# Optimization experiments

Measured on AMD Instinct MI355X. Metric: run time of the kernel, lower is better.

The kernel has to match this reference:

```python
import jax, jax.numpy as jnp
import numpy as np

N_NODES = 65536
N_EDGES = 1048576
VOCAB = 50000
HIDDEN = 256
LAYERS = 3
NUM_GRAPHS = 64
NEG_SLOPE = 0.2  # PyG GATConv default LeakyReLU slope
EPS = 1e-16      # PyG softmax denominator epsilon


def setup_inputs() -> dict:
    key = jax.random.key(0)
    ks = jax.random.split(key, 12)
    s = 0.02
    nodes = jax.random.randint(ks[0], (N_NODES,), 0, VOCAB, dtype=jnp.int32)
    edge_index = jax.random.randint(ks[1], (2, N_EDGES), 0, N_NODES, dtype=jnp.int32)
    batch = jnp.sort(jax.random.randint(ks[2], (N_NODES,), 0, NUM_GRAPHS, dtype=jnp.int32))
    emb = jax.random.normal(ks[3], (VOCAB, HIDDEN), jnp.float32) * s
    Wg = jax.random.normal(ks[4], (LAYERS, HIDDEN, HIDDEN), jnp.float32) * s
    a_src = jax.random.normal(ks[5], (LAYERS, HIDDEN), jnp.float32) * s
    a_dst = jax.random.normal(ks[6], (LAYERS, HIDDEN), jnp.float32) * s
    bg = jnp.zeros((LAYERS, HIDDEN), jnp.float32)
    Wl = jax.random.normal(ks[7], (LAYERS, HIDDEN, HIDDEN), jnp.float32) * s
    bl = jnp.zeros((LAYERS, HIDDEN), jnp.float32)
    Wout = jax.random.normal(ks[8], (HIDDEN, VOCAB), jnp.float32) * s
    bout = jnp.zeros((VOCAB,), jnp.float32)
    return {"nodes": nodes, "edge_index": edge_index, "batch": batch,
            "emb": emb, "Wg": Wg, "a_src": a_src, "a_dst": a_dst, "bg": bg,
            "Wl": Wl, "bl": bl, "Wout": Wout, "bout": bout}


def _gat_layer(x, src, dst, W, a_s, a_d, b, n):
    h = x @ W                                    # [N, H]
    e = jax.nn.leaky_relu((h @ a_s)[src] + (h @ a_d)[dst], NEG_SLOPE)  # [E]
    m = jax.ops.segment_max(e, dst, num_segments=n)
    w = jnp.exp(e - m[dst])
    denom = jax.ops.segment_sum(w, dst, num_segments=n)
    alpha = w / (denom[dst] + EPS)               # segment softmax over incoming edges
    out = jax.ops.segment_sum(h[src] * alpha[:, None], dst, num_segments=n)
    return out + b


def reference(nodes, edge_index, batch, emb, Wg, a_src, a_dst, bg, Wl, bl, Wout, bout):
    n = nodes.shape[0]
    loop = jnp.arange(n, dtype=edge_index.dtype)  # GATConv add_self_loops=True
    src = jnp.concatenate([edge_index[0], loop])
    dst = jnp.concatenate([edge_index[1], loop])
    x = emb[nodes]                                # [N, H]
    for l in range(Wg.shape[0]):
        x = _gat_layer(x, src, dst, Wg[l], a_src[l], a_dst[l], bg[l], n)
        x = jax.nn.relu(x)
        x = x @ Wl[l] + bl[l]
    sums = jax.ops.segment_sum(x, batch, num_segments=NUM_GRAPHS)
    cnt = jax.ops.segment_sum(jnp.ones((n,), x.dtype), batch, num_segments=NUM_GRAPHS)
    pooled = sums / jnp.maximum(cnt, 1.0)[:, None]  # global mean pool -> [G, H]
    return pooled @ Wout + bout                      # [G, V]
```

## Files before the change

### kernel.cpp

```cpp
#include <hip/hip_runtime.h>

#define N_NODES 65536
#define N_EDGES 1048576
#define E_TOTAL (N_EDGES + N_NODES)
#define VOCAB 50000
#define HIDDEN 256
#define NUM_GRAPHS 64
#define NEG_SLOPE 0.2f
#define SM_EPS 1e-16f

#define NBKT 128
#define BKT_SHIFT 9
#define DSTS_PER_BKT 512
#define BKT_CAP 10240
#define EDGES_PER_BLK1 4352

typedef _Float16 f16x8 __attribute__((ext_vector_type(8)));
typedef _Float16 f16x4 __attribute__((ext_vector_type(4)));
typedef float f32x4 __attribute__((ext_vector_type(4)));

__global__ __launch_bounds__(256) void gather_kernel(const int* __restrict__ nodes,
    const float* __restrict__ emb, _Float16* __restrict__ x) {
    int i = blockIdx.x;
    int t = threadIdx.x;
    x[(size_t)i * HIDDEN + t] = (_Float16)emb[(size_t)nodes[i] * HIDDEN + t];
}

__global__ __launch_bounds__(256) void prep_wt_kernel(const float* __restrict__ Wg,
    const float* __restrict__ Wl, _Float16* __restrict__ WT) {
    int mat = blockIdx.y;
    int n = blockIdx.x;
    int k = threadIdx.x;
    float s;
    if (mat == 0) {
        s = Wg[(size_t)k * HIDDEN + n];
    } else {
        const float* A = Wl + (size_t)(mat - 1) * HIDDEN * HIDDEN;
        const float* B = Wg + (size_t)mat * HIDDEN * HIDDEN;
        s = 0.f;
        for (int j = 0; j < HIDDEN; j++)
            s += A[(size_t)k * HIDDEN + j] * B[(size_t)j * HIDDEN + n];
    }
    WT[(size_t)mat * HIDDEN * HIDDEN + (size_t)n * HIDDEN + k] = (_Float16)s;
}

__global__ __launch_bounds__(256) void fuse_b_kernel(const float* __restrict__ Wg,
    const float* __restrict__ bl, float* __restrict__ bfused) {
    int pair = blockIdx.x;
    int n = threadIdx.x;
    const float* B = Wg + (size_t)(pair + 1) * HIDDEN * HIDDEN;
    const float* b = bl + (size_t)pair * HIDDEN;
    float s = 0.f;
    for (int k = 0; k < HIDDEN; k++) s += b[k] * B[(size_t)k * HIDDEN + n];
    bfused[pair * HIDDEN + n] = s;
}

__global__ __launch_bounds__(256) void bucket_kernel(const int* __restrict__ ei,
    int* __restrict__ bcur, unsigned* __restrict__ staging) {
    __shared__ int lhist[NBKT];
    __shared__ int lbase[NBKT];
    __shared__ int lcur[NBKT];
    int tid = threadIdx.x;
    if (tid < NBKT) lhist[tid] = 0;
    __syncthreads();
    int e0 = blockIdx.x * EDGES_PER_BLK1;
    int mySrc[17], myDst[17];
    #pragma unroll
    for (int k = 0; k < 17; k++) {
        int e = e0 + k * 256 + tid;
        int src, dst;
        if (e < N_EDGES) { src = ei[e]; dst = ei[N_EDGES + e]; }
        else             { src = dst = e - N_EDGES; }
        mySrc[k] = src; myDst[k] = dst;
        atomicAdd(&lhist[dst >> BKT_SHIFT], 1);
    }
    __syncthreads();
    if (tid < NBKT) {
        int c = lhist[tid];
        lbase[tid] = (c > 0) ? atomicAdd(&bcur[tid], c) : 0;
        lcur[tid] = 0;
    }
    __syncthreads();
    #pragma unroll
    for (int k = 0; k < 17; k++) {
        int b = myDst[k] >> BKT_SHIFT;
        int pos = lbase[b] + atomicAdd(&lcur[b], 1);
        staging[(size_t)b * BKT_CAP + pos] =
            ((unsigned)(myDst[k] & (DSTS_PER_BKT - 1)) << 16) | (unsigned)mySrc[k];
    }
}

__global__ __launch_bounds__(256) void csr_kernel(const int* __restrict__ bcur,
    const unsigned* __restrict__ staging, int* __restrict__ row_ptr,
    int* __restrict__ src_sorted) {
    __shared__ unsigned sedge[BKT_CAP];
    __shared__ int shist[DSTS_PER_BKT];
    __shared__ int sbase[DSTS_PER_BKT];
    __shared__ int spart[256];
    int b = blockIdx.x;
    int tid = threadIdx.x;
    int cnt = bcur[b];

    spart[tid] = (tid < NBKT && tid < b) ? bcur[tid] : 0;
    __syncthreads();
    for (int d = 128; d > 0; d >>= 1) {
        if (tid < d) spart[tid] += spart[tid + d];
        __syncthreads();
    }
    int base = spart[0];
    __syncthreads();

    shist[tid] = 0; shist[tid + 256] = 0;
    __syncthreads();
    for (int i = tid; i < cnt; i += 256) {
        unsigned v = staging[(size_t)b * BKT_CAP + i];
        sedge[i] = v;
        atomicAdd(&shist[v >> 16], 1);
    }
    __syncthreads();
    int p = shist[2 * tid] + shist[2 * tid + 1];
    spart[tid] = p;
    __syncthreads();
    for (int d = 1; d < 256; d <<= 1) {
        int v = (tid >= d) ? spart[tid - d] : 0;
        __syncthreads();
        spart[tid] += v;
        __syncthreads();
    }
    int epair = spart[tid] - p;
    sbase[2 * tid] = epair;
    sbase[2 * tid + 1] = epair + shist[2 * tid];
    __syncthreads();
    row_ptr[b * DSTS_PER_BKT + tid] = base + sbase[tid];
    row_ptr[b * DSTS_PER_BKT + 256 + tid] = base + sbase[256 + tid];
    shist[tid] = sbase[tid];
    shist[tid + 256] = sbase[tid + 256];
    __syncthreads();
    for (int i = tid; i < cnt; i += 256) {
        unsigned v = sedge[i];
        int d = v >> 16;
        int pos = atomicAdd(&shist[d], 1);
        src_sorted[base + pos] = (int)(v & 0xFFFFu);
    }
    if (b == NBKT - 1 && tid == 0) row_ptr[N_NODES] = E_TOTAL;
}

#define PAD_K 40
template <bool FUSED>
__global__ __launch_bounds__(256) void gemm_f16_kernel(const _Float16* __restrict__ A,
    const _Float16* __restrict__ WT, const float* __restrict__ bias,
    _Float16* __restrict__ C,
    const float* __restrict__ a_s, const float* __restrict__ a_d,
    float* __restrict__ es, float* __restrict__ ed) {
    __shared__ _Float16 As[64][PAD_K];
    __shared__ _Float16 Bs[256][PAD_K];
    int tid = threadIdx.x;
    int wave = tid >> 6;
    int lane = tid & 63;
    int quad = lane >> 4;
    int l16 = lane & 15;
    int m0 = blockIdx.x * 64;

    f32x4 acc[16];
    #pragma unroll
    for (int ct = 0; ct < 16; ct++) acc[ct] = (f32x4){0.f, 0.f, 0.f, 0.f};

    for (int k0 = 0; k0 < HIDDEN; k0 += 32) {
        __syncthreads();
        {
            int row = tid >> 2, q = tid & 3;
            *(f16x8*)&As[row][q * 8] =
                *(const f16x8*)(A + (size_t)(m0 + row) * HIDDEN + k0 + q * 8);
        }
        #pragma unroll
        for (int i = 0; i < 4; i++) {
            int c = tid + i * 256;
            int row = c >> 2, q = c & 3;
            *(f16x8*)&Bs[row][q * 8] =
                *(const f16x8*)(WT + (size_t)row * HIDDEN + k0 + q * 8);
        }
        __syncthreads();
        f16x8 a = *(const f16x8*)&As[wave * 16 + l16][quad * 8];
        #pragma unroll
        for (int ct = 0; ct < 16; ct++) {
            f16x8 b = *(const f16x8*)&Bs[ct * 16 + l16][quad * 8];
            acc[ct] = __builtin_amdgcn_mfma_f32_16x16x32_f16(a, b, acc[ct], 0, 0, 0);
        }
    }
    int rowbase = m0 + wave * 16 + quad * 4;
    #pragma unroll
    for (int ct = 0; ct < 16; ct++) {
        int col = ct * 16 + l16;
        float bv = (bias != nullptr) ? bias[col] : 0.f;
        #pragma unroll
        for (int r = 0; r < 4; r++) {
            float hv = acc[ct][r] + bv;
            acc[ct][r] = hv;
            C[(size_t)(rowbase + r) * HIDDEN + col] = (_Float16)hv;
        }
    }
    if (FUSED) {
        float ds0 = 0.f, ds1 = 0.f, ds2 = 0.f, ds3 = 0.f;
        float dd0 = 0.f, dd1 = 0.f, dd2 = 0.f, dd3 = 0.f;
        #pragma unroll
        for (int ct = 0; ct < 16; ct++) {
            int col = ct * 16 + l16;
            float av = a_s[col];
            float dv = a_d[col];
            ds0 += acc[ct][0] * av; dd0 += acc[ct][0] * dv;
            ds1 += acc[ct][1] * av; dd1 += acc[ct][1] * dv;
            ds2 += acc[ct][2] * av; dd2 += acc[ct][2] * dv;
            ds3 += acc[ct][3] * av; dd3 += acc[ct][3] * dv;
        }
        #pragma unroll
        for (int off = 1; off < 16; off <<= 1) {
            ds0 += __shfl_xor(ds0, off); dd0 += __shfl_xor(dd0, off);
            ds1 += __shfl_xor(ds1, off); dd1 += __shfl_xor(dd1, off);
            ds2 += __shfl_xor(ds2, off); dd2 += __shfl_xor(dd2, off);
            ds3 += __shfl_xor(ds3, off); dd3 += __shfl_xor(dd3, off);
        }
        if (l16 == 0) {
            es[rowbase + 0] = ds0; ed[rowbase + 0] = dd0;
            es[rowbase + 1] = ds1; ed[rowbase + 1] = dd1;
            es[rowbase + 2] = ds2; ed[rowbase + 2] = dd2;
            es[rowbase + 3] = ds3; ed[rowbase + 3] = dd3;
        }
    }
}

__global__ __launch_bounds__(256) void agg_kernel(const _Float16* __restrict__ h,
    const int* __restrict__ row_ptr, const int* __restrict__ src_sorted,
    const float* __restrict__ es, const float* __restrict__ ed,
    const float* __restrict__ bg, _Float16* __restrict__ g) {
    int dst = blockIdx.x * 8 + (threadIdx.x >> 5);
    int l32 = threadIdx.x & 31;
    int start = row_ptr[dst];
    int end = row_ptr[dst + 1];
    float edd = ed[dst];
    const _Float16* hl = h + l32 * 8;

    float den0 = 0.f, den1 = 0.f;
    float acc[8];
    #pragma unroll
    for (int j = 0; j < 8; j++) acc[j] = 0.f;

    int i = start;
    for (; i + 7 < end; i += 8) {
        int s0 = src_sorted[i + 0];
        int s1 = src_sorted[i + 1];
        int s2 = src_sorted[i + 2];
        int s3 = src_sorted[i + 3];
        int s4 = src_sorted[i + 4];
        int s5 = src_sorted[i + 5];
        int s6 = src_sorted[i + 6];
        int s7 = src_sorted[i + 7];
        f16x8 r0 = *(const f16x8*)(hl + (unsigned)s0 * HIDDEN);
        f16x8 r1 = *(const f16x8*)(hl + (unsigned)s1 * HIDDEN);
        f16x8 r2 = *(const f16x8*)(hl + (unsigned)s2 * HIDDEN);
        f16x8 r3 = *(const f16x8*)(hl + (unsigned)s3 * HIDDEN);
        f16x8 r4 = *(const f16x8*)(hl + (unsigned)s4 * HIDDEN);
        f16x8 r5 = *(const f16x8*)(hl + (unsigned)s5 * HIDDEN);
        f16x8 r6 = *(const f16x8*)(hl + (unsigned)s6 * HIDDEN);
        f16x8 r7 = *(const f16x8*)(hl + (unsigned)s7 * HIDDEN);
        float e0 = es[s0] + edd; e0 = (e0 > 0.f) ? e0 : NEG_SLOPE * e0;
        float e1 = es[s1] + edd; e1 = (e1 > 0.f) ? e1 : NEG_SLOPE * e1;
        float e2 = es[s2] + edd; e2 = (e2 > 0.f) ? e2 : NEG_SLOPE * e2;
        float e3 = es[s3] + edd; e3 = (e3 > 0.f) ? e3 : NEG_SLOPE * e3;
        float e4 = es[s4] + edd; e4 = (e4 > 0.f) ? e4 : NEG_SLOPE * e4;
        float e5 = es[s5] + edd; e5 = (e5 > 0.f) ? e5 : NEG_SLOPE * e5;
        float e6 = es[s6] + edd; e6 = (e6 > 0.f) ? e6 : NEG_SLOPE * e6;
        float e7 = es[s7] + edd; e7 = (e7 > 0.f) ? e7 : NEG_SLOPE * e7;
        float w0 = __expf(e0);
        float w1 = __expf(e1);
        float w2 = __expf(e2);
        float w3 = __expf(e3);
        float w4 = __expf(e4);
        float w5 = __expf(e5);
        float w6 = __expf(e6);
        float w7 = __expf(e7);
        den0 += (w0 + w1) + (w2 + w3);
        den1 += (w4 + w5) + (w6 + w7);
        #pragma unroll
        for (int j = 0; j < 8; j++)
            acc[j] += (w0 * (float)r0[j] + w1 * (float)r1[j])
                    + (w2 * (float)r2[j] + w3 * (float)r3[j])
                    + (w4 * (float)r4[j] + w5 * (float)r5[j])
                    + (w6 * (float)r6[j] + w7 * (float)r7[j]);
    }
    for (; i + 3 < end; i += 4) {
        int s0 = src_sorted[i + 0];
        int s1 = src_sorted[i + 1];
        int s2 = src_sorted[i + 2];
        int s3 = src_sorted[i + 3];
        f16x8 r0 = *(const f16x8*)(hl + (unsigned)s0 * HIDDEN);
        f16x8 r1 = *(const f16x8*)(hl + (unsigned)s1 * HIDDEN);
        f16x8 r2 = *(const f16x8*)(hl + (unsigned)s2 * HIDDEN);
        f16x8 r3 = *(const f16x8*)(hl + (unsigned)s3 * HIDDEN);
        float e0 = es[s0] + edd; e0 = (e0 > 0.f) ? e0 : NEG_SLOPE * e0;
        float e1 = es[s1] + edd; e1 = (e1 > 0.f) ? e1 : NEG_SLOPE * e1;
        float e2 = es[s2] + edd; e2 = (e2 > 0.f) ? e2 : NEG_SLOPE * e2;
        float e3 = es[s3] + edd; e3 = (e3 > 0.f) ? e3 : NEG_SLOPE * e3;
        float w0 = __expf(e0);
        float w1 = __expf(e1);
        float w2 = __expf(e2);
        float w3 = __expf(e3);
        den0 += (w0 + w1) + (w2 + w3);
        #pragma unroll
        for (int j = 0; j < 8; j++)
            acc[j] += (w0 * (float)r0[j] + w1 * (float)r1[j])
                    + (w2 * (float)r2[j] + w3 * (float)r3[j]);
    }
    for (; i < end; i++) {
        int s0 = src_sorted[i];
        f16x8 r0 = *(const f16x8*)(hl + (unsigned)s0 * HIDDEN);
        float e0 = es[s0] + edd; e0 = (e0 > 0.f) ? e0 : NEG_SLOPE * e0;
        float w0 = __expf(e0);
        den1 += w0;
        #pragma unroll
        for (int j = 0; j < 8; j++) acc[j] += w0 * (float)r0[j];
    }

    float inv = 1.0f / ((den0 + den1) + SM_EPS);
    float4 b0 = *(const float4*)(bg + l32 * 8);
    float4 b1 = *(const float4*)(bg + l32 * 8 + 4);
    f16x8 outv;
    outv[0] = (_Float16)fmaxf(acc[0] * inv + b0.x, 0.f);
    outv[1] = (_Float16)fmaxf(acc[1] * inv + b0.y, 0.f);
    outv[2] = (_Float16)fmaxf(acc[2] * inv + b0.z, 0.f);
    outv[3] = (_Float16)fmaxf(acc[3] * inv + b0.w, 0.f);
    outv[4] = (_Float16)fmaxf(acc[4] * inv + b1.x, 0.f);
    outv[5] = (_Float16)fmaxf(acc[5] * inv + b1.y, 0.f);
    outv[6] = (_Float16)fmaxf(acc[6] * inv + b1.z, 0.f);
    outv[7] = (_Float16)fmaxf(acc[7] * inv + b1.w, 0.f);
    *(f16x8*)(g + (size_t)dst * HIDDEN + l32 * 8) = outv;
}

__global__ __launch_bounds__(128) void graph_bounds_kernel(const int* __restrict__ batch,
    int* __restrict__ gstart) {
    int g = threadIdx.x;
    if (g > NUM_GRAPHS) return;
    if (g == NUM_GRAPHS) { gstart[NUM_GRAPHS] = N_NODES; return; }
    int lo = 0, hi = N_NODES;
    while (lo < hi) {
        int mid = (lo + hi) >> 1;
        if (batch[mid] < g) lo = mid + 1; else hi = mid;
    }
    gstart[g] = lo;
}

#define POOL_SPLITS 16
__global__ __launch_bounds__(256) void pool_partial_kernel(const _Float16* __restrict__ x,
    const int* __restrict__ gstart, float* __restrict__ pooledT) {
    int g = blockIdx.x;
    int chunk = blockIdx.y;
    int t = threadIdx.x;
    int s = gstart[g];
    int e = gstart[g + 1];
    int n = e - s;
    int per = (n + POOL_SPLITS - 1) / POOL_SPLITS;
    int r0 = s + chunk * per;
    int r1 = min(r0 + per, e);
    if (r0 >= r1) return;
    float acc = 0.f;
    for (int r = r0; r < r1; r++) acc += (float)x[(size_t)r * HIDDEN + t];
    atomicAdd(&pooledT[t * NUM_GRAPHS + g], acc);
}

__global__ __launch_bounds__(256) void mean_kernel(const float* __restrict__ pooledT,
    const int* __restrict__ gstart, float* __restrict__ meanT) {
    int i = blockIdx.x * 256 + threadIdx.x;
    int g = i & (NUM_GRAPHS - 1);
    float c = (float)max(gstart[g + 1] - gstart[g], 1);
    meanT[i] = pooledT[i] / c;
}

__global__ __launch_bounds__(256) void wl2_kernel(const float* __restrict__ meanP,
    const float* __restrict__ Wl, const float* __restrict__ bl,
    float* __restrict__ meanT2) {
    int g = blockIdx.x;
    int n = threadIdx.x;
    const float* W2 = Wl + (size_t)2 * HIDDEN * HIDDEN;
    float s = bl[2 * HIDDEN + n];
    for (int k = 0; k < HIDDEN; k++)
        s += meanP[k * NUM_GRAPHS + g] * W2[(size_t)k * HIDDEN + n];
    meanT2[n * NUM_GRAPHS + g] = s;
}

__global__ __launch_bounds__(256) void final_kernel(const float* __restrict__ meanT,
    const float* __restrict__ Wout, const float* __restrict__ bout, float* __restrict__ out) {
    int j = blockIdx.x * 64 + (threadIdx.x & 63);
    int g0 = __builtin_amdgcn_readfirstlane((threadIdx.x >> 6) * 16);
    if (j >= VOCAB) return;
    float acc[16];
    #pragma unroll
    for (int g = 0; g < 16; g++) acc[g] = 0.f;
    #pragma unroll 4
    for (int k = 0; k < HIDDEN; k++) {
        float w = Wout[(size_t)k * VOCAB + j];
        const float* mrow = meanT + k * NUM_GRAPHS + g0;
        #pragma unroll
        for (int g = 0; g < 16; g++) acc[g] += mrow[g] * w;
    }
    float b = bout[j];
    #pragma unroll
    for (int g = 0; g < 16; g++) out[(size_t)(g0 + g) * VOCAB + j] = acc[g] + b;
}

extern "C" void kernel_launch(void* const* d_in, const int* in_sizes, int n_in,
                              void* d_out, int out_size, void* d_ws, size_t ws_size,
                              hipStream_t stream) {
    const int*   nodes = (const int*)d_in[0];
    const int*   ei    = (const int*)d_in[1];
    const int*   batch = (const int*)d_in[2];
    const float* emb   = (const float*)d_in[3];
    const float* Wg    = (const float*)d_in[4];
    const float* a_src = (const float*)d_in[5];
    const float* a_dst = (const float*)d_in[6];
    const float* bg    = (const float*)d_in[7];
    const float* Wl    = (const float*)d_in[8];
    const float* bl    = (const float*)d_in[9];
    const float* Wout  = (const float*)d_in[10];
    const float* bout  = (const float*)d_in[11];
    float* out = (float*)d_out;

    char* ws = (char*)d_ws;
    size_t off = 0;
    auto alloc = [&](size_t bytes) -> void* {
        void* p = ws + off;
        off += (bytes + 255) & ~(size_t)255;
        return p;
    };
    _Float16* bufA    = (_Float16*)alloc((size_t)N_NODES * HIDDEN * 2);
    _Float16* bufB    = (_Float16*)alloc((size_t)N_NODES * HIDDEN * 2);
    _Float16* WT      = (_Float16*)alloc((size_t)3 * HIDDEN * HIDDEN * 2);
    float* bfused     = (float*)alloc((size_t)2 * HIDDEN * 4);
    float* es         = (float*)alloc((size_t)N_NODES * 4);
    float* ed         = (float*)alloc((size_t)N_NODES * 4);
    int*   row_ptr    = (int*)alloc((size_t)(N_NODES + 1) * 4);
    int*   src_sorted = (int*)alloc((size_t)E_TOTAL * 4);
    int*   bcur       = (int*)alloc((size_t)NBKT * 4);
    unsigned* staging = (unsigned*)alloc((size_t)NBKT * BKT_CAP * 4);
    float* pooledT    = (float*)alloc((size_t)HIDDEN * NUM_GRAPHS * 4);
    float* meanT      = (float*)alloc((size_t)HIDDEN * NUM_GRAPHS * 4);
    float* meanT2     = (float*)alloc((size_t)HIDDEN * NUM_GRAPHS * 4);
    int*   gstart     = (int*)alloc((size_t)(NUM_GRAPHS + 1) * 4);

    hipMemsetAsync(bcur, 0, (size_t)NBKT * 4, stream);
    hipMemsetAsync(pooledT, 0, (size_t)HIDDEN * NUM_GRAPHS * 4, stream);

    prep_wt_kernel<<<dim3(HIDDEN, 3), 256, 0, stream>>>(Wg, Wl, WT);
    fuse_b_kernel<<<2, 256, 0, stream>>>(Wg, bl, bfused);
    gather_kernel<<<N_NODES, 256, 0, stream>>>(nodes, emb, bufA);
    bucket_kernel<<<E_TOTAL / EDGES_PER_BLK1, 256, 0, stream>>>(ei, bcur, staging);
    csr_kernel<<<NBKT, 256, 0, stream>>>(bcur, staging, row_ptr, src_sorted);

    for (int l = 0; l < 3; l++) {
        const float* bias = (l == 0) ? nullptr : (bfused + (size_t)(l - 1) * HIDDEN);
        gemm_f16_kernel<true><<<N_NODES / 64, 256, 0, stream>>>(
            bufA, WT + (size_t)l * HIDDEN * HIDDEN, bias, bufB,
            a_src + (size_t)l * HIDDEN, a_dst + (size_t)l * HIDDEN, es, ed);
        agg_kernel<<<N_NODES / 8, 256, 0, stream>>>(
            bufB, row_ptr, src_sorted, es, ed, bg + (size_t)l * HIDDEN, bufA);
    }

    graph_bounds_kernel<<<1, 128, 0, stream>>>(batch, gstart);
    pool_partial_kernel<<<dim3(NUM_GRAPHS, POOL_SPLITS), 256, 0, stream>>>(bufA, gstart, pooledT);
    mean_kernel<<<(HIDDEN * NUM_GRAPHS) / 256, 256, 0, stream>>>(pooledT, gstart, meanT);
    wl2_kernel<<<NUM_GRAPHS, 256, 0, stream>>>(meanT, Wl, bl, meanT2);
    final_kernel<<<dim3((VOCAB + 63) / 64), 256, 0, stream>>>(meanT2, Wout, bout, out);
}
```

Measured before the change: 675.8 us.

## Fuse embedding gather into first GEMM and enlarge GEMM tile to 128 rows

Removes the standalone gather kernel by having the layer-0 GEMM load embedding rows directly from the float table via the node indices and convert them to fp16 while staging into shared memory. The GEMM block grows to 512 threads covering 128 rows, so each weight tile staged in shared memory is reused by twice as many rows. This avoids writing and re-reading the gathered fp16 activation buffer. In exchange, the gather now uses scalar float loads inside the GEMM's K loop, and the larger blocks can change occupancy.

```diff
diff --git a/kernel.cpp b/kernel.cpp
--- a/kernel.cpp
+++ b/kernel.cpp
@@ -18,13 +18,6 @@
 typedef _Float16 f16x8 __attribute__((ext_vector_type(8)));
 typedef _Float16 f16x4 __attribute__((ext_vector_type(4)));
 typedef float f32x4 __attribute__((ext_vector_type(4)));
-
-__global__ __launch_bounds__(256) void gather_kernel(const int* __restrict__ nodes,
-    const float* __restrict__ emb, _Float16* __restrict__ x) {
-    int i = blockIdx.x;
-    int t = threadIdx.x;
-    x[(size_t)i * HIDDEN + t] = (_Float16)emb[(size_t)nodes[i] * HIDDEN + t];
-}
 
 __global__ __launch_bounds__(256) void prep_wt_kernel(const float* __restrict__ Wg,
     const float* __restrict__ Wl, _Float16* __restrict__ WT) {
@@ -146,20 +139,26 @@
 }
 
 #define PAD_K 40
-template <bool FUSED>
-__global__ __launch_bounds__(256) void gemm_f16_kernel(const _Float16* __restrict__ A,
+template <bool GATHER>
+__global__ __launch_bounds__(512) void gemm_f16_kernel(const _Float16* __restrict__ A,
+    const int* __restrict__ nodes, const float* __restrict__ emb,
     const _Float16* __restrict__ WT, const float* __restrict__ bias,
     _Float16* __restrict__ C,
     const float* __restrict__ a_s, const float* __restrict__ a_d,
     float* __restrict__ es, float* __restrict__ ed) {
-    __shared__ _Float16 As[64][PAD_K];
+    __shared__ _Float16 As[128][PAD_K];
     __shared__ _Float16 Bs[256][PAD_K];
+    __shared__ int snodes[128];
     int tid = threadIdx.x;
     int wave = tid >> 6;
     int lane = tid & 63;
     int quad = lane >> 4;
     int l16 = lane & 15;
-    int m0 = blockIdx.x * 64;
+    int m0 = blockIdx.x * 128;
+
+    if (GATHER) {
+        if (tid < 128) snodes[tid] = nodes[m0 + tid];
+    }
 
     f32x4 acc[16];
     #pragma unroll
@@ -169,12 +168,20 @@
         __syncthreads();
         {
             int row = tid >> 2, q = tid & 3;
-            *(f16x8*)&As[row][q * 8] =
-                *(const f16x8*)(A + (size_t)(m0 + row) * HIDDEN + k0 + q * 8);
-        }
-        #pragma unroll
-        for (int i = 0; i < 4; i++) {
-            int c = tid + i * 256;
+            if (GATHER) {
+                const float* src = emb + (size_t)snodes[row] * HIDDEN + k0 + q * 8;
+                f16x8 v;
+                #pragma unroll
+                for (int j = 0; j < 8; j++) v[j] = (_Float16)src[j];
+                *(f16x8*)&As[row][q * 8] = v;
+            } else {
+                *(f16x8*)&As[row][q * 8] =
+                    *(const f16x8*)(A + (size_t)(m0 + row) * HIDDEN + k0 + q * 8);
+            }
+        }
+        #pragma unroll
+        for (int i = 0; i < 2; i++) {
+            int c = tid + i * 512;
             int row = c >> 2, q = c & 3;
             *(f16x8*)&Bs[row][q * 8] =
                 *(const f16x8*)(WT + (size_t)row * HIDDEN + k0 + q * 8);
@@ -199,7 +206,7 @@
             C[(size_t)(rowbase + r) * HIDDEN + col] = (_Float16)hv;
         }
     }
-    if (FUSED) {
+    {
         float ds0 = 0.f, ds1 = 0.f, ds2 = 0.f, ds3 = 0.f;
         float dd0 = 0.f, dd1 = 0.f, dd2 = 0.f, dd3 = 0.f;
         #pragma unroll
@@ -450,15 +457,20 @@
 
     prep_wt_kernel<<<dim3(HIDDEN, 3), 256, 0, stream>>>(Wg, Wl, WT);
     fuse_b_kernel<<<2, 256, 0, stream>>>(Wg, bl, bfused);
-    gather_kernel<<<N_NODES, 256, 0, stream>>>(nodes, emb, bufA);
     bucket_kernel<<<E_TOTAL / EDGES_PER_BLK1, 256, 0, stream>>>(ei, bcur, staging);
     csr_kernel<<<NBKT, 256, 0, stream>>>(bcur, staging, row_ptr, src_sorted);
 
     for (int l = 0; l < 3; l++) {
         const float* bias = (l == 0) ? nullptr : (bfused + (size_t)(l - 1) * HIDDEN);
-        gemm_f16_kernel<true><<<N_NODES / 64, 256, 0, stream>>>(
-            bufA, WT + (size_t)l * HIDDEN * HIDDEN, bias, bufB,
-            a_src + (size_t)l * HIDDEN, a_dst + (size_t)l * HIDDEN, es, ed);
+        if (l == 0) {
+            gemm_f16_kernel<true><<<N_NODES / 128, 512, 0, stream>>>(
+                nullptr, nodes, emb, WT, nullptr, bufB,
+                a_src, a_dst, es, ed);
+        } else {
+            gemm_f16_kernel<false><<<N_NODES / 128, 512, 0, stream>>>(
+                bufA, nullptr, nullptr, WT + (size_t)l * HIDDEN * HIDDEN, bias, bufB,
+                a_src + (size_t)l * HIDDEN, a_dst + (size_t)l * HIDDEN, es, ed);
+        }
         agg_kernel<<<N_NODES / 8, 256, 0, stream>>>(
             bufB, row_ptr, src_sorted, es, ed, bg + (size_t)l * HIDDEN, bufA);
     }
```

New measurement: 620.9 us. -8.1%, faster.
